# Optimization experiments

Hardware: AMD Instinct MI355X
Metric: run time of the kernel (lower is better)

The kernel has to match this reference:

```python
import jax, jax.numpy as jnp
import numpy as np

B, U, CV, IN, H = 256, 64, 61, 3, 1024
NG, NAG = 20, 10
G = 4 * H  # LSTM gate width (i,f,g,o)


def _lstm_cell(x, h, c, Wih, Whh, bih, bhh):
    # PyTorch LSTM gate order: i, f, g, o
    g = x @ Wih.T + h @ Whh.T + bih + bhh
    i, f, gg, o = jnp.split(g, 4, axis=-1)
    c2 = jax.nn.sigmoid(f) * c + jax.nn.sigmoid(i) * jnp.tanh(gg)
    h2 = jax.nn.sigmoid(o) * jnp.tanh(c2)
    return h2, c2


def _bilstm(x, h, c, pf, pb):
    # Bidirectional LSTM over a length-1 sequence: one cell step per direction.
    hf, cf = _lstm_cell(x, h[0], c[0], *pf)
    hb, cb = _lstm_cell(x, h[1], c[1], *pb)
    return jnp.concatenate([hf, hb], axis=-1), jnp.stack([hf, hb]), jnp.stack([cf, cb])


def _forward(inp, char_vec, old_k, old_w, h1, c1, h2, c2, params, text_len):
    (Wih1f, Whh1f, bih1f, bhh1f, Wih1b, Whh1b, bih1b, bhh1b,
     Wih2f, Whh2f, bih2f, bhh2f, Wih2b, Whh2b, bih2b, bhh2b,
     W_win, b_win, W_mdn, b_mdn) = params
    # embed = cat([inp, old_w]) over the feature dim; seq len is 1 so squeeze it.
    x1 = jnp.concatenate([inp[:, 0], old_w[:, 0]], axis=-1)          # [B, IN+CV]
    out1, h1n, c1n = _bilstm(x1, h1, c1,
                             (Wih1f, Whh1f, bih1f, bhh1f),
                             (Wih1b, Whh1b, bih1b, bhh1b))           # [B, 2H]
    # Gaussian-mixture attention window (Graves 2013)
    abk = jnp.exp(out1 @ W_win.T + b_win)                            # [B, 3*NAG]
    a_t, b_t, k_t = jnp.split(abk, 3, axis=1)
    k_t = old_k + k_t
    u = jnp.arange(1, U + 1, dtype=jnp.float32)                      # [U]
    phi_bku = jnp.exp(-b_t[:, :, None] * (k_t[:, :, None] - u) ** 2) # [B,NAG,U]
    phi = jnp.einsum('bk,bku->bu', a_t, phi_bku) * (float(U) / text_len)
    win = jnp.einsum('bu,buc->bc', phi, char_vec)                    # [B, CV]
    # Second LSTM with skip connections
    x2 = jnp.concatenate([out1, inp[:, 0], win], axis=-1)            # [B, 2H+IN+CV]
    out2, h2n, c2n = _bilstm(x2, h2, c2,
                             (Wih2f, Whh2f, bih2f, bhh2f),
                             (Wih2b, Whh2b, bih2b, bhh2b))           # [B, 2H]
    # Mixture-density output head
    y = jnp.concatenate([out1, out2], axis=-1) @ W_mdn.T + b_mdn     # [B, 6*NG+1]
    e = jax.nn.sigmoid(y[:, :1])
    pi, mu1, mu2, s1, s2, rho = jnp.split(y[:, 1:], 6, axis=1)
    pi = jax.nn.softmax(pi, axis=1)  # bias = 0 default
    return (e, pi, mu1, mu2, jnp.exp(s1), jnp.exp(s2), jnp.tanh(rho),
            phi, win, k_t, h1n, c1n, h2n, c2n)


def setup_inputs() -> dict:
    key = jax.random.key(0)
    ks = jax.random.split(key, 32)
    def w(k, shape):
        return jax.random.normal(k, shape, dtype=jnp.float32) * 0.02
    d = {
        'inp': jax.random.normal(ks[0], (B, 1, IN), dtype=jnp.float32),
        'char_vec': jax.random.uniform(ks[1], (B, U, CV), dtype=jnp.float32),
        'old_k': jax.random.uniform(ks[2], (B, NAG), dtype=jnp.float32),
        'old_w': jax.random.uniform(ks[3], (B, 1, CV), dtype=jnp.float32),
        'h1': jnp.zeros((2, B, H), jnp.float32),
        'c1': jnp.zeros((2, B, H), jnp.float32),
        'h2': jnp.zeros((2, B, H), jnp.float32),
        'c2': jnp.zeros((2, B, H), jnp.float32),
        'text_len': 64,
    }
    in1 = IN + CV          # rnn1 input width = 64
    in2 = 2 * H + IN + CV  # rnn2 input width = 2112
    i = 4
    for pre, ind in [('1f', in1), ('1b', in1), ('2f', in2), ('2b', in2)]:
        d['Wih' + pre] = w(ks[i], (G, ind)); i += 1
        d['Whh' + pre] = w(ks[i], (G, H)); i += 1
        d['bih' + pre] = w(ks[i], (G,)); i += 1
        d['bhh' + pre] = w(ks[i], (G,)); i += 1
    d['W_win'] = w(ks[i], (3 * NAG, 2 * H)); i += 1
    d['b_win'] = w(ks[i], (3 * NAG,)) - 2.0; i += 1  # keep exp(abk) moderate
    d['W_mdn'] = w(ks[i], (6 * NG + 1, 4 * H)); i += 1
    d['b_mdn'] = w(ks[i], (6 * NG + 1,))
    return d


def reference(inp, char_vec, old_k, old_w, h1, c1, h2, c2, text_len,
              Wih1f, Whh1f, bih1f, bhh1f, Wih1b, Whh1b, bih1b, bhh1b,
              Wih2f, Whh2f, bih2f, bhh2f, Wih2b, Whh2b, bih2b, bhh2b,
              W_win, b_win, W_mdn, b_mdn):
    params = (Wih1f, Whh1f, bih1f, bhh1f, Wih1b, Whh1b, bih1b, bhh1b,
              Wih2f, Whh2f, bih2f, bhh2f, Wih2b, Whh2b, bih2b, bhh2b,
              W_win, b_win, W_mdn, b_mdn)
    return _forward(inp, char_vec, old_k, old_w, h1, c1, h2, c2, params, text_len)
```

## Files before the change

### kernel.cpp

```cpp
#include <hip/hip_runtime.h>

#define Bsz 256
#define Usz 64
#define CVsz 61
#define INsz 3
#define Hsz 1024
#define Gsz 4096
#define NGsz 20
#define NAGsz 10
#define IN2sz 2112

typedef __attribute__((ext_vector_type(8))) short bf16x8;
typedef __attribute__((ext_vector_type(4))) float f32x4;
typedef __attribute__((ext_vector_type(4))) unsigned int u32x4;

__device__ __forceinline__ unsigned int pk2(float x, float y) {
  unsigned int a = __float_as_uint(x), b = __float_as_uint(y);
  return ((a + 0x8000u) >> 16) | ((b + 0x8000u) & 0xffff0000u);
}
__device__ __forceinline__ unsigned short bf1(float x) {
  return (unsigned short)((__float_as_uint(x) + 0x8000u) >> 16);
}
__device__ __forceinline__ bf16x8 pkb(float4 lo, float4 hi) {
  union { u32x4 u; bf16x8 b; } cv;
  cv.u = (u32x4){pk2(lo.x, lo.y), pk2(lo.z, lo.w), pk2(hi.x, hi.y), pk2(hi.z, hi.w)};
  return cv.b;
}
__device__ __forceinline__ float sigf(float x) { return 1.f / (1.f + __expf(-x)); }

struct GemmP {
  const unsigned short* X1; int ldx1; int nc1;
  const unsigned short* Hst;
  const float* Wf1; const float* Wb1; int ldw1;
  const float* Wf2; const float* Wb2;
  const float* bihf; const float* bhhf; const float* bihb; const float* bhhb;
  float* gout;
  int ksplit; int totc; int ndir; int nW; int ldo;
};

__global__ __launch_bounds__(256) void gemm_k(GemmP p) {
  int t = threadIdx.x;
  int n0 = blockIdx.x * 128, m0 = blockIdx.y * 128;
  int z = blockIdx.z;
  int d = (p.ndir == 2) ? (z & 1) : 0;
  int s = (p.ndir == 2) ? (z >> 1) : z;
  const float* Wih = d ? p.Wb1 : p.Wf1;
  const float* Whh = d ? p.Wb2 : p.Wf2;
  const unsigned short* Hx = p.Hst + (size_t)d * Bsz * Hsz;
  int c0 = (p.totc * s) / p.ksplit, c1 = (p.totc * (s + 1)) / p.ksplit;
  int wv = t >> 6, ln = t & 63;
  int wr = wv >> 1, wc = wv & 1;
  int fr = ln & 15, kg = ln >> 4;

  int rA[4], rB[4];
#pragma unroll
  for (int i = 0; i < 4; i++) rA[i] = m0 + wr * 64 + i * 16 + fr;
#pragma unroll
  for (int j = 0; j < 4; j++) {
    int r = n0 + wc * 64 + j * 16 + fr;
    rB[j] = (r < p.nW) ? r : (p.nW - 1);
  }

  f32x4 acc[4][4];
#pragma unroll
  for (int i = 0; i < 4; i++)
#pragma unroll
    for (int j = 0; j < 4; j++) acc[i][j] = (f32x4){0.f, 0.f, 0.f, 0.f};

  int e1 = (c1 < p.nc1) ? c1 : p.nc1;
#pragma unroll 2
  for (int c = c0; c < e1; ++c) {
    int kx = c * 32 + kg * 8;
    bf16x8 av[4], bv[4];
#pragma unroll
    for (int i = 0; i < 4; i++)
      av[i] = *(const bf16x8*)(p.X1 + (size_t)rA[i] * p.ldx1 + kx);
#pragma unroll
    for (int j = 0; j < 4; j++) {
      const float* wp = Wih + (size_t)rB[j] * p.ldw1 + kx;
      bv[j] = pkb(*(const float4*)wp, *(const float4*)(wp + 4));
    }
#pragma unroll
    for (int i = 0; i < 4; i++)
#pragma unroll
      for (int j = 0; j < 4; j++)
        acc[i][j] = __builtin_amdgcn_mfma_f32_16x16x32_bf16(av[i], bv[j], acc[i][j], 0, 0, 0);
  }

  int s2 = (c0 > p.nc1) ? c0 : p.nc1;
#pragma unroll 2
  for (int c = s2; c < c1; ++c) {
    int kx = (c - p.nc1) * 32 + kg * 8;
    bf16x8 av[4], bv[4];
#pragma unroll
    for (int i = 0; i < 4; i++)
      av[i] = *(const bf16x8*)(Hx + (size_t)rA[i] * Hsz + kx);
#pragma unroll
    for (int j = 0; j < 4; j++) {
      const float* wp = Whh + (size_t)rB[j] * Hsz + kx;
      bv[j] = pkb(*(const float4*)wp, *(const float4*)(wp + 4));
    }
#pragma unroll
    for (int i = 0; i < 4; i++)
#pragma unroll
      for (int j = 0; j < 4; j++)
        acc[i][j] = __builtin_amdgcn_mfma_f32_16x16x32_bf16(av[i], bv[j], acc[i][j], 0, 0, 0);
  }

  const float* bi = d ? p.bihb : p.bihf;
  const float* bh = d ? p.bhhb : p.bhhf;
  float* outp = p.gout + (size_t)(s * p.ndir + d) * Bsz * p.ldo;
#pragma unroll
  for (int i = 0; i < 4; i++) {
#pragma unroll
    for (int j = 0; j < 4; j++) {
      int col = n0 + wc * 64 + j * 16 + fr;
      float bias = 0.f;
      if (p.bihf && s == 0) bias = bi[col] + bh[col];
#pragma unroll
      for (int r = 0; r < 4; r++) {
        int row = m0 + wr * 64 + i * 16 + kg * 4 + r;
        outp[(size_t)row * p.ldo + col] = acc[i][j][r] + bias;
      }
    }
  }
}

__global__ __launch_bounds__(256) void prep_x1b(const float* inp, const float* oldw, unsigned short* x1b) {
  int idx = blockIdx.x * 256 + threadIdx.x;
  int m = idx >> 6, k = idx & 63;
  float v = (k < INsz) ? inp[m * INsz + k] : oldw[m * CVsz + (k - INsz)];
  x1b[idx] = bf1(v);
}

__global__ __launch_bounds__(256) void cvt_h(const float* h, unsigned short* hb, int n) {
  int idx = blockIdx.x * 256 + threadIdx.x;
  if (idx < n) hb[idx] = bf1(h[idx]);
}

__global__ __launch_bounds__(256) void cell_k(const float* gates, int ksplit,
    const float* cin, float* hout, float* cout,
    unsigned short* db1, int ld1, int off1, unsigned short* db2, int ld2, int off2) {
  int idx = blockIdx.x * 256 + threadIdx.x;
  int j = idx & (Hsz - 1);
  int m = (idx >> 10) & 255;
  int d = idx >> 18;
  size_t base = ((size_t)d * Bsz + m) * Gsz + j;
  float gi = 0.f, gf = 0.f, gg = 0.f, go = 0.f;
  for (int s = 0; s < ksplit; ++s) {
    const float* gp = gates + (size_t)s * 2 * Bsz * Gsz + base;
    gi += gp[0]; gf += gp[1024]; gg += gp[2048]; go += gp[3072];
  }
  float c = cin[((size_t)d * Bsz + m) * Hsz + j];
  float cn = sigf(gf) * c + sigf(gi) * tanhf(gg);
  float hn = sigf(go) * tanhf(cn);
  hout[((size_t)d * Bsz + m) * Hsz + j] = hn;
  cout[((size_t)d * Bsz + m) * Hsz + j] = cn;
  unsigned short hb = bf1(hn);
  db1[(size_t)m * ld1 + off1 + d * Hsz + j] = hb;
  if (db2) db2[(size_t)m * ld2 + off2 + d * Hsz + j] = hb;
}

__global__ __launch_bounds__(128) void win_fin(const float* winp, int ks,
    const float* bwin, const float* oldk, const float* inp, const float* cvec,
    const int* tl, unsigned short* x2b, float* ophi, float* owin, float* okt) {
  int m = blockIdx.x, t = threadIdx.x, wv = t >> 6, ln = t & 63;
  __shared__ float abk[30];
  __shared__ float phis[Usz];
  __shared__ float wpart[2][CVsz];
  if (t < 30) {
    float s = bwin[t];
    for (int q = 0; q < ks; ++q) s += winp[((size_t)q * Bsz + m) * 128 + t];
    abk[t] = __expf(s);
  }
  __syncthreads();
  if (t < NAGsz) {
    float kt = oldk[m * NAGsz + t] + abk[20 + t];
    abk[20 + t] = kt;
    okt[m * NAGsz + t] = kt;
  }
  __syncthreads();
  if (t < Usz) {
    float scale = 64.f / (float)tl[0];
    float ph = 0.f;
#pragma unroll
    for (int q = 0; q < NAGsz; ++q) {
      float dk = abk[20 + q] - (float)(t + 1);
      ph += abk[q] * __expf(-abk[10 + q] * dk * dk);
    }
    ph *= scale;
    phis[t] = ph;
    ophi[m * Usz + t] = ph;
  }
  __syncthreads();
  if (ln < CVsz) {
    float w = 0.f;
    const float* cv = cvec + (size_t)m * Usz * CVsz + (size_t)wv * 32 * CVsz + ln;
#pragma unroll
    for (int u = 0; u < 32; ++u) w += phis[wv * 32 + u] * cv[u * CVsz];
    wpart[wv][ln] = w;
  }
  __syncthreads();
  if (t < CVsz) {
    float w = wpart[0][t] + wpart[1][t];
    owin[m * CVsz + t] = w;
    x2b[(size_t)m * IN2sz + 2048 + INsz + t] = bf1(w);
  }
  if (t < INsz) x2b[(size_t)m * IN2sz + 2048 + t] = bf1(inp[m * INsz + t]);
}

__global__ __launch_bounds__(128) void mdn_fin(const float* part, int ks, const float* bm, float* out) {
  int m = blockIdx.x, t = threadIdx.x;
  __shared__ float y[121];
  if (t < 121) {
    float s = bm[t];
    for (int q = 0; q < ks; ++q) s += part[((size_t)q * Bsz + m) * 128 + t];
    y[t] = s;
  }
  __syncthreads();
  if (t == 0) out[m] = sigf(y[0]);
  if (t < NGsz) {
    float mx = -1e30f;
    for (int q = 0; q < NGsz; q++) mx = fmaxf(mx, y[1 + q]);
    float se = 0.f;
    for (int q = 0; q < NGsz; q++) se += __expf(y[1 + q] - mx);
    out[256   + m * NGsz + t] = __expf(y[1 + t] - mx) / se;
    out[5376  + m * NGsz + t] = y[21 + t];
    out[10496 + m * NGsz + t] = y[41 + t];
    out[15616 + m * NGsz + t] = __expf(y[61 + t]);
    out[20736 + m * NGsz + t] = __expf(y[81 + t]);
    out[25856 + m * NGsz + t] = tanhf(y[101 + t]);
  }
}

extern "C" void kernel_launch(void* const* d_in, const int* in_sizes, int n_in,
                              void* d_out, int out_size, void* d_ws, size_t ws_size,
                              hipStream_t stream) {
  (void)in_sizes; (void)n_in; (void)out_size;
  const float* inp  = (const float*)d_in[0];
  const float* cvec = (const float*)d_in[1];
  const float* oldk = (const float*)d_in[2];
  const float* oldw = (const float*)d_in[3];
  const float* h1   = (const float*)d_in[4];
  const float* c1   = (const float*)d_in[5];
  const float* h2   = (const float*)d_in[6];
  const float* c2   = (const float*)d_in[7];
  const int*   tl   = (const int*)d_in[8];
  float* out = (float*)d_out;
  float* ws  = (float*)d_ws;

  size_t fixed_f = (size_t)524288 + 524288 + 8192 + 262144 + 262144 + 270336 + 524288;
  int ks2 = 4;
  while (ks2 > 1 && (fixed_f + (size_t)ks2 * 2 * 1048576) * 4 > ws_size) ks2 >>= 1;
  int ks1 = 4;

  float* ws_g    = ws;
  float* ws_mdn  = ws_g + (size_t)ks2 * 2 * 1048576;
  float* ws_winp = ws_mdn + 524288;
  float* bstart  = ws_winp + 524288;
  unsigned short* x1b  = (unsigned short*)bstart;
  unsigned short* h1b  = x1b + 16384;
  unsigned short* h2b  = h1b + 524288;
  unsigned short* x2b  = h2b + 524288;
  unsigned short* catb = x2b + 540672;

  prep_x1b<<<64, 256, 0, stream>>>(inp, oldw, x1b);
  cvt_h<<<2048, 256, 0, stream>>>(h1, h1b, 524288);
  cvt_h<<<2048, 256, 0, stream>>>(h2, h2b, 524288);

  GemmP g1{};
  g1.X1 = x1b; g1.ldx1 = 64; g1.nc1 = 2;
  g1.Hst = h1b;
  g1.Wf1 = (const float*)d_in[9];  g1.Wb1 = (const float*)d_in[13]; g1.ldw1 = 64;
  g1.Wf2 = (const float*)d_in[10]; g1.Wb2 = (const float*)d_in[14];
  g1.bihf = (const float*)d_in[11]; g1.bhhf = (const float*)d_in[12];
  g1.bihb = (const float*)d_in[15]; g1.bhhb = (const float*)d_in[16];
  g1.gout = ws_g; g1.ksplit = ks1; g1.totc = 34; g1.ndir = 2; g1.nW = 4096; g1.ldo = 4096;
  gemm_k<<<dim3(32, 2, 2 * ks1), 256, 0, stream>>>(g1);

  cell_k<<<2048, 256, 0, stream>>>(ws_g, ks1, c1, out + 65536, out + 589824,
                                   x2b, IN2sz, 0, catb, 4096, 0);

  GemmP gw{};
  gw.X1 = x2b; gw.ldx1 = IN2sz; gw.nc1 = 64;
  gw.Hst = x2b;
  gw.Wf1 = (const float*)d_in[25]; gw.Wb1 = (const float*)d_in[25]; gw.ldw1 = 2048;
  gw.Wf2 = (const float*)d_in[25]; gw.Wb2 = (const float*)d_in[25];
  gw.bihf = nullptr; gw.bhhf = nullptr; gw.bihb = nullptr; gw.bhhb = nullptr;
  gw.gout = ws_winp; gw.ksplit = 16; gw.totc = 64; gw.ndir = 1; gw.nW = 30; gw.ldo = 128;
  gemm_k<<<dim3(1, 2, 16), 256, 0, stream>>>(gw);

  win_fin<<<256, 128, 0, stream>>>(ws_winp, 16, (const float*)d_in[26],
                                   oldk, inp, cvec, tl, x2b,
                                   out + 30976, out + 47360, out + 62976);

  GemmP g2{};
  g2.X1 = x2b; g2.ldx1 = IN2sz; g2.nc1 = 66;
  g2.Hst = h2b;
  g2.Wf1 = (const float*)d_in[17]; g2.Wb1 = (const float*)d_in[21]; g2.ldw1 = IN2sz;
  g2.Wf2 = (const float*)d_in[18]; g2.Wb2 = (const float*)d_in[22];
  g2.bihf = (const float*)d_in[19]; g2.bhhf = (const float*)d_in[20];
  g2.bihb = (const float*)d_in[23]; g2.bhhb = (const float*)d_in[24];
  g2.gout = ws_g; g2.ksplit = ks2; g2.totc = 98; g2.ndir = 2; g2.nW = 4096; g2.ldo = 4096;
  gemm_k<<<dim3(32, 2, 2 * ks2), 256, 0, stream>>>(g2);

  cell_k<<<2048, 256, 0, stream>>>(ws_g, ks2, c2, out + 1114112, out + 1638400,
                                   catb, 4096, 2048, nullptr, 0, 0);

  GemmP gm{};
  gm.X1 = catb; gm.ldx1 = 4096; gm.nc1 = 128;
  gm.Hst = catb;
  gm.Wf1 = (const float*)d_in[27]; gm.Wb1 = (const float*)d_in[27]; gm.ldw1 = 4096;
  gm.Wf2 = (const float*)d_in[27]; gm.Wb2 = (const float*)d_in[27];
  gm.bihf = nullptr; gm.bhhf = nullptr; gm.bihb = nullptr; gm.bhhb = nullptr;
  gm.gout = ws_mdn; gm.ksplit = 16; gm.totc = 128; gm.ndir = 1; gm.nW = 121; gm.ldo = 128;
  gemm_k<<<dim3(1, 2, 16), 256, 0, stream>>>(gm);

  mdn_fin<<<256, 128, 0, stream>>>(ws_mdn, 16, (const float*)d_in[28], out);
}
```

Measured before the change: 348.7 us.

## Stage GEMM tiles through LDS with async direct loads and double buffering

The LSTM gate GEMM now copies A (bf16) and W (fp32) tiles into double-buffered shared memory using global_load_lds direct-to-LDS loads, with XOR swizzling so the MFMA operand reads avoid bank conflicts. Loading the next K-chunk overlaps with computing the current one, where before each wave issued scattered per-lane global loads. This trades roughly 48KB of LDS per block, which can lower occupancy, and adds a barrier per K step. The workspace size formula is also recomputed and ks1 now follows ks2.

```diff
diff --git a/kernel.cpp b/kernel.cpp
--- a/kernel.cpp
+++ b/kernel.cpp
@@ -21,12 +21,18 @@
 __device__ __forceinline__ unsigned short bf1(float x) {
   return (unsigned short)((__float_as_uint(x) + 0x8000u) >> 16);
 }
-__device__ __forceinline__ bf16x8 pkb(float4 lo, float4 hi) {
+__device__ __forceinline__ bf16x8 pkb4(f32x4 lo, f32x4 hi) {
   union { u32x4 u; bf16x8 b; } cv;
-  cv.u = (u32x4){pk2(lo.x, lo.y), pk2(lo.z, lo.w), pk2(hi.x, hi.y), pk2(hi.z, hi.w)};
+  cv.u = (u32x4){pk2(lo[0], lo[1]), pk2(lo[2], lo[3]), pk2(hi[0], hi[1]), pk2(hi[2], hi[3])};
   return cv.b;
 }
 __device__ __forceinline__ float sigf(float x) { return 1.f / (1.f + __expf(-x)); }
+
+__device__ __forceinline__ void gload16(const void* g, void* l) {
+  __builtin_amdgcn_global_load_lds(
+      (const __attribute__((address_space(1))) unsigned int*)g,
+      (__attribute__((address_space(3))) unsigned int*)l, 16, 0, 0);
+}
 
 struct GemmP {
   const unsigned short* X1; int ldx1; int nc1;
@@ -39,6 +45,8 @@
 };
 
 __global__ __launch_bounds__(256) void gemm_k(GemmP p) {
+  __shared__ __align__(16) unsigned short Alds[2][128 * 32];
+  __shared__ __align__(16) float Wlds[2][128 * 32];
   int t = threadIdx.x;
   int n0 = blockIdx.x * 128, m0 = blockIdx.y * 128;
   int z = blockIdx.z;
@@ -52,60 +60,65 @@
   int wr = wv >> 1, wc = wv & 1;
   int fr = ln & 15, kg = ln >> 4;
 
-  int rA[4], rB[4];
-#pragma unroll
-  for (int i = 0; i < 4; i++) rA[i] = m0 + wr * 64 + i * 16 + fr;
-#pragma unroll
-  for (int j = 0; j < 4; j++) {
-    int r = n0 + wc * 64 + j * 16 + fr;
-    rB[j] = (r < p.nW) ? r : (p.nW - 1);
-  }
-
   f32x4 acc[4][4];
 #pragma unroll
   for (int i = 0; i < 4; i++)
 #pragma unroll
     for (int j = 0; j < 4; j++) acc[i][j] = (f32x4){0.f, 0.f, 0.f, 0.f};
 
-  int e1 = (c1 < p.nc1) ? c1 : p.nc1;
-#pragma unroll 2
-  for (int c = c0; c < e1; ++c) {
-    int kx = c * 32 + kg * 8;
+  auto STAGE = [&](int buf, int c) {
+    const unsigned short* Xp; int ldx; const float* Wp; int ldw; int kx;
+    if (c < p.nc1) { Xp = p.X1; ldx = p.ldx1; kx = c * 32; Wp = Wih; ldw = p.ldw1; }
+    else           { Xp = Hx;   ldx = Hsz;    kx = (c - p.nc1) * 32; Wp = Whh; ldw = Hsz; }
+#pragma unroll
+    for (int q = 0; q < 2; q++) {
+      int r0 = (wv * 2 + q) * 16;
+      int row = r0 + (ln >> 2);
+      int ch = (ln & 3) ^ ((row >> 1) & 3);
+      gload16(Xp + (size_t)(m0 + row) * ldx + kx + ch * 8, &Alds[buf][r0 * 32]);
+    }
+#pragma unroll
+    for (int q = 0; q < 4; q++) {
+      int r0 = (wv * 4 + q) * 8;
+      int row = r0 + (ln >> 3);
+      int rw = n0 + row; if (rw >= p.nW) rw = p.nW - 1;
+      int ch = (ln & 7) ^ (row & 7);
+      gload16(Wp + (size_t)rw * ldw + kx + ch * 4, &Wlds[buf][r0 * 32]);
+    }
+  };
+
+  auto COMPUTE = [&](int buf) {
     bf16x8 av[4], bv[4];
-#pragma unroll
-    for (int i = 0; i < 4; i++)
-      av[i] = *(const bf16x8*)(p.X1 + (size_t)rA[i] * p.ldx1 + kx);
+    int gA = (fr >> 1) & 3, gW = fr & 7;
+#pragma unroll
+    for (int i = 0; i < 4; i++) {
+      int row = wr * 64 + i * 16 + fr;
+      av[i] = *(const bf16x8*)&Alds[buf][row * 32 + (kg ^ gA) * 8];
+    }
 #pragma unroll
     for (int j = 0; j < 4; j++) {
-      const float* wp = Wih + (size_t)rB[j] * p.ldw1 + kx;
-      bv[j] = pkb(*(const float4*)wp, *(const float4*)(wp + 4));
+      int row = wc * 64 + j * 16 + fr;
+      f32x4 lo = *(const f32x4*)&Wlds[buf][row * 32 + ((2 * kg) ^ gW) * 4];
+      f32x4 hi = *(const f32x4*)&Wlds[buf][row * 32 + ((2 * kg + 1) ^ gW) * 4];
+      bv[j] = pkb4(lo, hi);
     }
 #pragma unroll
     for (int i = 0; i < 4; i++)
 #pragma unroll
       for (int j = 0; j < 4; j++)
         acc[i][j] = __builtin_amdgcn_mfma_f32_16x16x32_bf16(av[i], bv[j], acc[i][j], 0, 0, 0);
-  }
-
-  int s2 = (c0 > p.nc1) ? c0 : p.nc1;
-#pragma unroll 2
-  for (int c = s2; c < c1; ++c) {
-    int kx = (c - p.nc1) * 32 + kg * 8;
-    bf16x8 av[4], bv[4];
-#pragma unroll
-    for (int i = 0; i < 4; i++)
-      av[i] = *(const bf16x8*)(Hx + (size_t)rA[i] * Hsz + kx);
-#pragma unroll
-    for (int j = 0; j < 4; j++) {
-      const float* wp = Whh + (size_t)rB[j] * Hsz + kx;
-      bv[j] = pkb(*(const float4*)wp, *(const float4*)(wp + 4));
-    }
-#pragma unroll
-    for (int i = 0; i < 4; i++)
-#pragma unroll
-      for (int j = 0; j < 4; j++)
-        acc[i][j] = __builtin_amdgcn_mfma_f32_16x16x32_bf16(av[i], bv[j], acc[i][j], 0, 0, 0);
-  }
+  };
+
+  STAGE(0, c0);
+  __syncthreads();
+  int cur = 0;
+  for (int c = c0 + 1; c < c1; ++c) {
+    STAGE(cur ^ 1, c);
+    COMPUTE(cur);
+    __syncthreads();
+    cur ^= 1;
+  }
+  COMPUTE(cur);
 
   const float* bi = d ? p.bihb : p.bihf;
   const float* bh = d ? p.bhhb : p.bhhf;
@@ -249,10 +262,10 @@
   float* out = (float*)d_out;
   float* ws  = (float*)d_ws;
 
-  size_t fixed_f = (size_t)524288 + 524288 + 8192 + 262144 + 262144 + 270336 + 524288;
+  size_t fixed_f = (size_t)524288 + 524288 + 1327104;
   int ks2 = 4;
   while (ks2 > 1 && (fixed_f + (size_t)ks2 * 2 * 1048576) * 4 > ws_size) ks2 >>= 1;
-  int ks1 = 4;
+  int ks1 = ks2;
 
   float* ws_g    = ws;
   float* ws_mdn  = ws_g + (size_t)ks2 * 2 * 1048576;
```

Result: faster. 299.5 us (-14.1%).
